# Kernel optimization log

Measured on AMD Instinct MI355X. Metric: run time of the kernel, lower is better.

The kernel has to match this reference:

```python
import jax, jax.numpy as jnp
import numpy as np

NEG = -1.0e9

def setup_inputs() -> dict:
    key = jax.random.key(0)
    kq, kk, kv = jax.random.split(key, 3)
    B, Sq, Sk, D = 8, 2048, 2048, 128
    q = jax.random.normal(kq, (B, Sq, D), dtype=jnp.float32)
    k = jax.random.normal(kk, (B, Sk, D), dtype=jnp.float32)
    v = jax.random.normal(kv, (B, Sk, D), dtype=jnp.float32)
    mask = jnp.ones((B, Sq, Sk), dtype=jnp.int32)  # 1 = attend
    return {"q": q, "k": k, "v": v, "mask": mask}

def reference(q, k, v, mask):
    # scaled scores: [B, Sq, Sk]
    temper = jnp.sqrt(jnp.asarray(k.shape[-1], dtype=q.dtype))
    attn = jnp.einsum('bqd,bkd->bqk', q, k) / temper
    # additive mask: -1e9 where mask == 0
    attn = attn + NEG * (1.0 - mask.astype(attn.dtype))
    attn = jax.nn.softmax(attn, axis=-1)
    # dropout rate 0.0 -> identity
    out = jnp.einsum('bqk,bkd->bqd', attn, v)
    return out, attn
```

## Files before the change

kernel.cpp:

```cpp
#include <hip/hip_runtime.h>
#include <hip/hip_bf16.h>

#define BB 8
#define SQ 2048
#define SK 2048
#define DD 128
#define INV_TEMPER 0.08838834764831845f

using s16x8 = __attribute__((ext_vector_type(8))) short;
using f32x4 = __attribute__((ext_vector_type(4))) float;

__device__ __forceinline__ unsigned short f2bf(float f) {
  union { float f; unsigned u; } v; v.f = f;
  unsigned r = v.u + 0x7FFFu + ((v.u >> 16) & 1u);
  return (unsigned short)(r >> 16);
}
__device__ __forceinline__ float bf2f(unsigned short h) {
  union { unsigned u; float f; } v; v.u = ((unsigned)h) << 16; return v.f;
}
__device__ __forceinline__ void bar_lds() {
  asm volatile("s_waitcnt lgkmcnt(0)" ::: "memory");
  __builtin_amdgcn_s_barrier();
}

__global__ __launch_bounds__(256) void prep_k_kernel(const float* __restrict__ k,
                                                     unsigned short* __restrict__ kb) {
  const size_t i = ((size_t)blockIdx.x * 256 + threadIdx.x) * 8;
  const float4 a = *(const float4*)(k + i);
  const float4 c = *(const float4*)(k + i + 4);
  ushort4 o0, o1;
  o0.x = f2bf(a.x); o0.y = f2bf(a.y); o0.z = f2bf(a.z); o0.w = f2bf(a.w);
  o1.x = f2bf(c.x); o1.y = f2bf(c.y); o1.z = f2bf(c.z); o1.w = f2bf(c.w);
  *(ushort4*)(kb + i) = o0;
  *(ushort4*)(kb + i + 4) = o1;
}

__global__ __launch_bounds__(256) void prep_v_kernel(const float* __restrict__ v,
                                                     unsigned short* __restrict__ vt) {
  constexpr int TS = 132;
  __shared__ __align__(16) unsigned short tile[64 * TS];
  const int tid = threadIdx.x;
  const int bid = blockIdx.x;
  const int b  = bid >> 5;
  const int k0 = (bid & 31) << 6;
#pragma unroll
  for (int p = 0; p < 8; ++p) {
    const int row = p * 8 + (tid >> 5);
    const int c4  = (tid & 31) << 2;
    const float4 vv = *(const float4*)(v + ((size_t)(b * SK + k0 + row)) * DD + c4);
    ushort4 o; o.x = f2bf(vv.x); o.y = f2bf(vv.y); o.z = f2bf(vv.z); o.w = f2bf(vv.w);
    *(ushort4*)(&tile[row * TS + c4]) = o;
  }
  __syncthreads();
#pragma unroll
  for (int p = 0; p < 8; ++p) {
    const int u = p * 256 + tid;
    const int d  = u >> 4;
    const int kw = (u & 15) << 2;
    ushort4 o;
    o.x = tile[(kw + 0) * TS + d];
    o.y = tile[(kw + 1) * TS + d];
    o.z = tile[(kw + 2) * TS + d];
    o.w = tile[(kw + 3) * TS + d];
    *(ushort4*)(vt + ((size_t)(b * DD + d)) * SK + k0 + kw) = o;
  }
}

__global__ __launch_bounds__(512, 4) void fused_attn(
    const float* __restrict__ q, const int* __restrict__ mask,
    const unsigned short* __restrict__ kb, const unsigned short* __restrict__ vt,
    float* __restrict__ outp, float* __restrict__ attn) {
  constexpr int BMS = 260;
  constexpr int LDP = 136;
  __shared__ unsigned char bm[32 * BMS];
  __shared__ __align__(16) unsigned short p_lds[2][32][LDP];
  __shared__ float redl[8][32];

  const int tid = threadIdx.x;
  const int bid = blockIdx.x;
  const int swz = ((bid & 7) << 6) + (bid >> 3);
  const int b  = swz >> 6;
  const int q0 = (swz & 63) << 5;
  const int lane = tid & 63;
  const int w    = tid >> 6;
  const int lrow = lane & 15;
  const int lk   = lane >> 4;
  const int colw = (w << 4) + lrow;
  const int cbyte = colw >> 3;
  const int cbit  = colw & 7;
  const int rowb  = lk << 2;

  {
    const int* mbase = mask + ((size_t)(b * SQ + q0)) * SK;
#pragma unroll
    for (int i = 0; i < 16; ++i) {
      const int u = (i << 9) + tid;
      const int grow = u >> 8;
      const int gb   = u & 255;
      const int* pp = mbase + (size_t)grow * SK + ((size_t)gb << 3);
      const int4 m0 = *(const int4*)pp;
      const int4 m1 = *(const int4*)(pp + 4);
      unsigned bv = (unsigned)(m0.x != 0) | ((unsigned)(m0.y != 0) << 1) |
                    ((unsigned)(m0.z != 0) << 2) | ((unsigned)(m0.w != 0) << 3) |
                    ((unsigned)(m1.x != 0) << 4) | ((unsigned)(m1.y != 0) << 5) |
                    ((unsigned)(m1.z != 0) << 6) | ((unsigned)(m1.w != 0) << 7);
      bm[grow * BMS + gb] = (unsigned char)bv;
    }
  }

  s16x8 af0[4], af1[4];
#pragma unroll
  for (int ks = 0; ks < 4; ++ks) {
    const float* qp0 = q + ((size_t)(b * SQ + q0 + lrow)) * DD + ks * 32 + lk * 8;
    const float* qp1 = qp0 + 16 * DD;
    const float4 a0 = *(const float4*)qp0;
    const float4 a1 = *(const float4*)(qp0 + 4);
    const float4 c0 = *(const float4*)qp1;
    const float4 c1 = *(const float4*)(qp1 + 4);
    s16x8 x, y;
    x[0] = (short)f2bf(a0.x); x[1] = (short)f2bf(a0.y); x[2] = (short)f2bf(a0.z); x[3] = (short)f2bf(a0.w);
    x[4] = (short)f2bf(a1.x); x[5] = (short)f2bf(a1.y); x[6] = (short)f2bf(a1.z); x[7] = (short)f2bf(a1.w);
    y[0] = (short)f2bf(c0.x); y[1] = (short)f2bf(c0.y); y[2] = (short)f2bf(c0.z); y[3] = (short)f2bf(c0.w);
    y[4] = (short)f2bf(c1.x); y[5] = (short)f2bf(c1.y); y[6] = (short)f2bf(c1.z); y[7] = (short)f2bf(c1.w);
    af0[ks] = x; af1[ks] = y;
  }

  const unsigned short* kbb = kb + (size_t)b * SK * DD + (size_t)colw * DD + lk * 8;

  bar_lds();

  float ls[8];
#pragma unroll
  for (int i = 0; i < 8; ++i) ls[i] = 0.0f;

  s16x8 bA[4], bB[4];
#pragma unroll
  for (int ks = 0; ks < 4; ++ks) bA[ks] = *(const s16x8*)(kbb + ks * 32);

  auto qk_sink1 = [&](int t, const f32x4& a0, const f32x4& a1) {
    const int bybase = (t << 4) + cbyte;
#pragma unroll
    for (int rt = 0; rt < 2; ++rt)
#pragma unroll
      for (int r = 0; r < 4; ++r) {
        const int row = rt * 16 + rowb + r;
        const int live = (bm[row * BMS + bybase] >> cbit) & 1;
        const float s = (rt ? a1[r] : a0[r]) * INV_TEMPER;
        ls[rt * 4 + r] += live ? __expf(s) : 0.0f;
      }
  };
  auto qk_mfma = [&](const s16x8* bf, f32x4& a0, f32x4& a1) {
    __builtin_amdgcn_s_setprio(1);
#pragma unroll
    for (int ks = 0; ks < 4; ++ks) {
      a0 = __builtin_amdgcn_mfma_f32_16x16x32_bf16(af0[ks], bf[ks], a0, 0, 0, 0);
      a1 = __builtin_amdgcn_mfma_f32_16x16x32_bf16(af1[ks], bf[ks], a1, 0, 0, 0);
    }
    __builtin_amdgcn_s_setprio(0);
  };

#pragma unroll 1
  for (int tp = 0; tp < 8; ++tp) {
    const int t0 = tp << 1, t1 = t0 + 1;
    {
      const unsigned short* p = kbb + (size_t)t1 * (128 * DD);
#pragma unroll
      for (int ks = 0; ks < 4; ++ks) bB[ks] = *(const s16x8*)(p + ks * 32);
    }
    f32x4 a0 = {0.f,0.f,0.f,0.f}, a1 = {0.f,0.f,0.f,0.f};
    qk_mfma(bA, a0, a1);
    qk_sink1(t0, a0, a1);
    {
      const int tn = (t0 + 2) & 15;
      const unsigned short* p = kbb + (size_t)tn * (128 * DD);
#pragma unroll
      for (int ks = 0; ks < 4; ++ks) bA[ks] = *(const s16x8*)(p + ks * 32);
    }
    f32x4 c0 = {0.f,0.f,0.f,0.f}, c1 = {0.f,0.f,0.f,0.f};
    qk_mfma(bB, c0, c1);
    qk_sink1(t1, c0, c1);
  }

#pragma unroll
  for (int i = 0; i < 8; ++i) {
    float l = ls[i];
#pragma unroll
    for (int d = 1; d < 16; d <<= 1) l += __shfl_xor(l, d);
    ls[i] = l;
  }
  if (lrow == 0) {
#pragma unroll
    for (int i = 0; i < 8; ++i) redl[w][(i >> 2) * 16 + rowb + (i & 3)] = ls[i];
  }
#pragma unroll
  for (int ks = 0; ks < 4; ++ks) bA[ks] = *(const s16x8*)(kbb + ks * 32);
  bar_lds();
  float il[8];
#pragma unroll
  for (int i = 0; i < 8; ++i) {
    const int row = (i >> 2) * 16 + rowb + (i & 3);
    float l = 0.0f;
#pragma unroll
    for (int ww = 0; ww < 8; ++ww) l += redl[ww][row];
    il[i] = 1.0f / l;
  }

  f32x4 o0 = {0.f,0.f,0.f,0.f}, o1 = {0.f,0.f,0.f,0.f};
  const unsigned short* vrow = vt + ((size_t)(b * DD + colw)) * SK + lk * 8;
  const int arow  = tid >> 4;
  const int acol0 = (tid & 15) << 3;
  float* attn_base = attn + ((size_t)(b * SQ + q0 + arow)) * SK + acol0;

  auto pv_iter = [&](int t, const s16x8* bcur, s16x8* bnx) {
    const int kr0 = t << 7;
    const int buf = t & 1;
    {
      const int tn = (t + 1) & 15;
      const unsigned short* p = kbb + (size_t)tn * (128 * DD);
#pragma unroll
      for (int ks = 0; ks < 4; ++ks) bnx[ks] = *(const s16x8*)(p + ks * 32);
    }
    s16x8 vf[4];
#pragma unroll
    for (int ks = 0; ks < 4; ++ks) vf[ks] = *(const s16x8*)(vrow + kr0 + ks * 32);
    f32x4 a0 = {0.f,0.f,0.f,0.f}, a1 = {0.f,0.f,0.f,0.f};
    qk_mfma(bcur, a0, a1);
    const int bybase = (t << 4) + cbyte;
#pragma unroll
    for (int rt = 0; rt < 2; ++rt)
#pragma unroll
      for (int r = 0; r < 4; ++r) {
        const int row = rt * 16 + rowb + r;
        const int live = (bm[row * BMS + bybase] >> cbit) & 1;
        const float s = (rt ? a1[r] : a0[r]) * INV_TEMPER;
        const float p = live ? __expf(s) * il[rt * 4 + r] : 0.0f;
        p_lds[buf][row][colw] = f2bf(p);
      }
    bar_lds();
    {
      const s16x8 pr = *(const s16x8*)(&p_lds[buf][arow][acol0]);
      float4 g0, g1;
      g0.x = bf2f((unsigned short)pr[0]); g0.y = bf2f((unsigned short)pr[1]);
      g0.z = bf2f((unsigned short)pr[2]); g0.w = bf2f((unsigned short)pr[3]);
      g1.x = bf2f((unsigned short)pr[4]); g1.y = bf2f((unsigned short)pr[5]);
      g1.z = bf2f((unsigned short)pr[6]); g1.w = bf2f((unsigned short)pr[7]);
      *(float4*)(attn_base + kr0) = g0;
      *(float4*)(attn_base + kr0 + 4) = g1;
    }
    __builtin_amdgcn_s_setprio(1);
#pragma unroll
    for (int ks = 0; ks < 4; ++ks) {
      const s16x8 pa0 = *(const s16x8*)(&p_lds[buf][lrow][ks * 32 + lk * 8]);
      const s16x8 pa1 = *(const s16x8*)(&p_lds[buf][16 + lrow][ks * 32 + lk * 8]);
      o0 = __builtin_amdgcn_mfma_f32_16x16x32_bf16(pa0, vf[ks], o0, 0, 0, 0);
      o1 = __builtin_amdgcn_mfma_f32_16x16x32_bf16(pa1, vf[ks], o1, 0, 0, 0);
    }
    __builtin_amdgcn_s_setprio(0);
  };

#pragma unroll 1
  for (int tp = 0; tp < 8; ++tp) {
    pv_iter((tp << 1),     bA, bB);
    pv_iter((tp << 1) + 1, bB, bA);
  }

#pragma unroll
  for (int rt = 0; rt < 2; ++rt)
#pragma unroll
    for (int r = 0; r < 4; ++r) {
      const int row = q0 + rt * 16 + rowb + r;
      outp[((size_t)(b * SQ + row)) * DD + colw] = (rt ? o1[r] : o0[r]);
    }
}

extern "C" void kernel_launch(void* const* d_in, const int* in_sizes, int n_in,
                              void* d_out, int out_size, void* d_ws, size_t ws_size,
                              hipStream_t stream) {
  const float* q = (const float*)d_in[0];
  const float* k = (const float*)d_in[1];
  const float* v = (const float*)d_in[2];
  const int* mask = (const int*)d_in[3];
  float* outp = (float*)d_out;
  float* attn = outp + (size_t)BB * SQ * DD;

  unsigned short* kb = (unsigned short*)d_ws;
  unsigned short* vt = kb + (size_t)BB * SK * DD;

  prep_k_kernel<<<(BB * SK * DD) / (256 * 8), 256, 0, stream>>>(k, kb);
  prep_v_kernel<<<BB * (SK / 64), 256, 0, stream>>>(v, vt);
  fused_attn<<<BB * (SQ / 32), 512, 0, stream>>>(q, mask, kb, vt, outp, attn);
}
```

Measured before the change: 140.7 us.

## Single-pass attention: store unnormalized P in LDS, split keys across waves

Replaces the two-pass scheme (sum of exponentials first, then recomputing QK^T for PV) with a single pass. Each wave owns a 256-key slice, writes unnormalized bf16 exp scores into a full 32x2048 LDS buffer and accumulates partial PV products. The partial outputs are reduced across waves with LDS atomics and normalized at the end, and the attention matrix is written from LDS with nontemporal stores. This removes the second QK^T matmul and the per-tile barriers. In exchange it needs much more LDS, so occupancy drops (launch bounds lowered to 2), and it relies on exp without max subtraction and on LDS float atomics.

Result: slower. 245.0 us (+74.1%).

```diff
diff --git a/kernel.cpp b/kernel.cpp
--- a/kernel.cpp
+++ b/kernel.cpp
@@ -9,6 +9,7 @@
 
 using s16x8 = __attribute__((ext_vector_type(8))) short;
 using f32x4 = __attribute__((ext_vector_type(4))) float;
+using i32x4 = __attribute__((ext_vector_type(4))) int;
 
 __device__ __forceinline__ unsigned short f2bf(float f) {
   union { float f; unsigned u; } v; v.f = f;
@@ -17,10 +18,6 @@
 }
 __device__ __forceinline__ float bf2f(unsigned short h) {
   union { unsigned u; float f; } v; v.u = ((unsigned)h) << 16; return v.f;
-}
-__device__ __forceinline__ void bar_lds() {
-  asm volatile("s_waitcnt lgkmcnt(0)" ::: "memory");
-  __builtin_amdgcn_s_barrier();
 }
 
 __global__ __launch_bounds__(256) void prep_k_kernel(const float* __restrict__ k,
@@ -66,15 +63,18 @@
   }
 }
 
-__global__ __launch_bounds__(512, 4) void fused_attn(
+#define PSTR 2056
+#define BMS  260
+
+__global__ __launch_bounds__(512, 2) void fused_attn(
     const float* __restrict__ q, const int* __restrict__ mask,
     const unsigned short* __restrict__ kb, const unsigned short* __restrict__ vt,
     float* __restrict__ outp, float* __restrict__ attn) {
-  constexpr int BMS = 260;
-  constexpr int LDP = 136;
+  __shared__ __align__(16) unsigned short P[32 * PSTR];
   __shared__ unsigned char bm[32 * BMS];
-  __shared__ __align__(16) unsigned short p_lds[2][32][LDP];
+  __shared__ float obuf[32 * 128];
   __shared__ float redl[8][32];
+  __shared__ float il_s[32];
 
   const int tid = threadIdx.x;
   const int bid = blockIdx.x;
@@ -85,10 +85,11 @@
   const int w    = tid >> 6;
   const int lrow = lane & 15;
   const int lk   = lane >> 4;
-  const int colw = (w << 4) + lrow;
-  const int cbyte = colw >> 3;
-  const int cbit  = colw & 7;
-  const int rowb  = lk << 2;
+  const int rowb = lk << 2;
+  const int slice0 = w << 8;
+
+#pragma unroll
+  for (int i = 0; i < 8; ++i) obuf[tid + (i << 9)] = 0.0f;
 
   {
     const int* mbase = mask + ((size_t)(b * SQ + q0)) * SK;
@@ -98,8 +99,8 @@
       const int grow = u >> 8;
       const int gb   = u & 255;
       const int* pp = mbase + (size_t)grow * SK + ((size_t)gb << 3);
-      const int4 m0 = *(const int4*)pp;
-      const int4 m1 = *(const int4*)(pp + 4);
+      const i32x4 m0 = __builtin_nontemporal_load((const i32x4*)pp);
+      const i32x4 m1 = __builtin_nontemporal_load(((const i32x4*)pp) + 1);
       unsigned bv = (unsigned)(m0.x != 0) | ((unsigned)(m0.y != 0) << 1) |
                     ((unsigned)(m0.z != 0) << 2) | ((unsigned)(m0.w != 0) << 3) |
                     ((unsigned)(m1.x != 0) << 4) | ((unsigned)(m1.y != 0) << 5) |
@@ -125,60 +126,73 @@
     af0[ks] = x; af1[ks] = y;
   }
 
-  const unsigned short* kbb = kb + (size_t)b * SK * DD + (size_t)colw * DD + lk * 8;
-
-  bar_lds();
+  __syncthreads();
+
+  const unsigned short* kfp = kb + (size_t)b * SK * DD + (size_t)(slice0 + lrow) * DD + lk * 8;
+  const unsigned short* vfp = vt + ((size_t)(b * DD + lrow)) * SK + slice0 + lk * 8;
 
   float ls[8];
 #pragma unroll
   for (int i = 0; i < 8; ++i) ls[i] = 0.0f;
-
-  s16x8 bA[4], bB[4];
-#pragma unroll
-  for (int ks = 0; ks < 4; ++ks) bA[ks] = *(const s16x8*)(kbb + ks * 32);
-
-  auto qk_sink1 = [&](int t, const f32x4& a0, const f32x4& a1) {
-    const int bybase = (t << 4) + cbyte;
+  f32x4 oA[8], oB[8];
+#pragma unroll
+  for (int nt = 0; nt < 8; ++nt) { oA[nt] = f32x4{0.f,0.f,0.f,0.f}; oB[nt] = f32x4{0.f,0.f,0.f,0.f}; }
+
+  auto qk_sink = [&](int ct, const s16x8* kf) {
+    f32x4 a0 = {0.f,0.f,0.f,0.f}, a1 = {0.f,0.f,0.f,0.f};
+    __builtin_amdgcn_s_setprio(1);
+#pragma unroll
+    for (int ks = 0; ks < 4; ++ks) {
+      a0 = __builtin_amdgcn_mfma_f32_16x16x32_bf16(af0[ks], kf[ks], a0, 0, 0, 0);
+      a1 = __builtin_amdgcn_mfma_f32_16x16x32_bf16(af1[ks], kf[ks], a1, 0, 0, 0);
+    }
+    __builtin_amdgcn_s_setprio(0);
+    const int colg = slice0 + (ct << 4) + lrow;
+    const int byb = colg >> 3, bit = colg & 7;
 #pragma unroll
     for (int rt = 0; rt < 2; ++rt)
 #pragma unroll
       for (int r = 0; r < 4; ++r) {
         const int row = rt * 16 + rowb + r;
-        const int live = (bm[row * BMS + bybase] >> cbit) & 1;
+        const int live = (bm[row * BMS + byb] >> bit) & 1;
         const float s = (rt ? a1[r] : a0[r]) * INV_TEMPER;
-        ls[rt * 4 + r] += live ? __expf(s) : 0.0f;
+        const float e = live ? __expf(s) : 0.0f;
+        ls[rt * 4 + r] += e;
+        P[row * PSTR + colg] = f2bf(e);
       }
   };
-  auto qk_mfma = [&](const s16x8* bf, f32x4& a0, f32x4& a1) {
+
+  s16x8 kA[4], kB[4];
+#pragma unroll
+  for (int ks = 0; ks < 4; ++ks) kA[ks] = *(const s16x8*)(kfp + ks * 32);
+
+#pragma unroll 1
+  for (int kk = 0; kk < 8; ++kk) {
+    const int koff = kk << 5;
+    s16x8 vf[8];
+#pragma unroll
+    for (int nt = 0; nt < 8; ++nt)
+      vf[nt] = *(const s16x8*)(vfp + (size_t)(nt << 4) * SK + koff);
+#pragma unroll
+    for (int ks = 0; ks < 4; ++ks)
+      kB[ks] = *(const s16x8*)(kfp + (size_t)(((kk << 1) + 1) << 4) * DD + ks * 32);
+    qk_sink(kk << 1, kA);
+#pragma unroll
+    for (int ks = 0; ks < 4; ++ks)
+      kA[ks] = *(const s16x8*)(kfp + (size_t)((((kk << 1) + 2) & 15) << 4) * DD + ks * 32);
+    qk_sink((kk << 1) + 1, kB);
+    asm volatile("s_waitcnt lgkmcnt(0)" ::: "memory");
+    __builtin_amdgcn_sched_barrier(0);
+    const int ko = slice0 + koff + (lk << 3);
+    const s16x8 pa0 = *(const s16x8*)(&P[lrow * PSTR + ko]);
+    const s16x8 pa1 = *(const s16x8*)(&P[(16 + lrow) * PSTR + ko]);
     __builtin_amdgcn_s_setprio(1);
 #pragma unroll
-    for (int ks = 0; ks < 4; ++ks) {
-      a0 = __builtin_amdgcn_mfma_f32_16x16x32_bf16(af0[ks], bf[ks], a0, 0, 0, 0);
-      a1 = __builtin_amdgcn_mfma_f32_16x16x32_bf16(af1[ks], bf[ks], a1, 0, 0, 0);
+    for (int nt = 0; nt < 8; ++nt) {
+      oA[nt] = __builtin_amdgcn_mfma_f32_16x16x32_bf16(pa0, vf[nt], oA[nt], 0, 0, 0);
+      oB[nt] = __builtin_amdgcn_mfma_f32_16x16x32_bf16(pa1, vf[nt], oB[nt], 0, 0, 0);
     }
     __builtin_amdgcn_s_setprio(0);
-  };
-
-#pragma unroll 1
-  for (int tp = 0; tp < 8; ++tp) {
-    const int t0 = tp << 1, t1 = t0 + 1;
-    {
-      const unsigned short* p = kbb + (size_t)t1 * (128 * DD);
-#pragma unroll
-      for (int ks = 0; ks < 4; ++ks) bB[ks] = *(const s16x8*)(p + ks * 32);
-    }
-    f32x4 a0 = {0.f,0.f,0.f,0.f}, a1 = {0.f,0.f,0.f,0.f};
-    qk_mfma(bA, a0, a1);
-    qk_sink1(t0, a0, a1);
-    {
-      const int tn = (t0 + 2) & 15;
-      const unsigned short* p = kbb + (size_t)tn * (128 * DD);
-#pragma unroll
-      for (int ks = 0; ks < 4; ++ks) bA[ks] = *(const s16x8*)(p + ks * 32);
-    }
-    f32x4 c0 = {0.f,0.f,0.f,0.f}, c1 = {0.f,0.f,0.f,0.f};
-    qk_mfma(bB, c0, c1);
-    qk_sink1(t1, c0, c1);
   }
 
 #pragma unroll
@@ -190,87 +204,53 @@
   }
   if (lrow == 0) {
 #pragma unroll
-    for (int i = 0; i < 8; ++i) redl[w][(i >> 2) * 16 + rowb + (i & 3)] = ls[i];
-  }
-#pragma unroll
-  for (int ks = 0; ks < 4; ++ks) bA[ks] = *(const s16x8*)(kbb + ks * 32);
-  bar_lds();
-  float il[8];
-#pragma unroll
-  for (int i = 0; i < 8; ++i) {
-    const int row = (i >> 2) * 16 + rowb + (i & 3);
-    float l = 0.0f;
-#pragma unroll
-    for (int ww = 0; ww < 8; ++ww) l += redl[ww][row];
-    il[i] = 1.0f / l;
-  }
-
-  f32x4 o0 = {0.f,0.f,0.f,0.f}, o1 = {0.f,0.f,0.f,0.f};
-  const unsigned short* vrow = vt + ((size_t)(b * DD + colw)) * SK + lk * 8;
-  const int arow  = tid >> 4;
-  const int acol0 = (tid & 15) << 3;
-  float* attn_base = attn + ((size_t)(b * SQ + q0 + arow)) * SK + acol0;
-
-  auto pv_iter = [&](int t, const s16x8* bcur, s16x8* bnx) {
-    const int kr0 = t << 7;
-    const int buf = t & 1;
-    {
-      const int tn = (t + 1) & 15;
-      const unsigned short* p = kbb + (size_t)tn * (128 * DD);
-#pragma unroll
-      for (int ks = 0; ks < 4; ++ks) bnx[ks] = *(const s16x8*)(p + ks * 32);
-    }
-    s16x8 vf[4];
-#pragma unroll
-    for (int ks = 0; ks < 4; ++ks) vf[ks] = *(const s16x8*)(vrow + kr0 + ks * 32);
-    f32x4 a0 = {0.f,0.f,0.f,0.f}, a1 = {0.f,0.f,0.f,0.f};
-    qk_mfma(bcur, a0, a1);
-    const int bybase = (t << 4) + cbyte;
-#pragma unroll
-    for (int rt = 0; rt < 2; ++rt)
-#pragma unroll
-      for (int r = 0; r < 4; ++r) {
-        const int row = rt * 16 + rowb + r;
-        const int live = (bm[row * BMS + bybase] >> cbit) & 1;
-        const float s = (rt ? a1[r] : a0[r]) * INV_TEMPER;
-        const float p = live ? __expf(s) * il[rt * 4 + r] : 0.0f;
-        p_lds[buf][row][colw] = f2bf(p);
-      }
-    bar_lds();
-    {
-      const s16x8 pr = *(const s16x8*)(&p_lds[buf][arow][acol0]);
-      float4 g0, g1;
-      g0.x = bf2f((unsigned short)pr[0]); g0.y = bf2f((unsigned short)pr[1]);
-      g0.z = bf2f((unsigned short)pr[2]); g0.w = bf2f((unsigned short)pr[3]);
-      g1.x = bf2f((unsigned short)pr[4]); g1.y = bf2f((unsigned short)pr[5]);
-      g1.z = bf2f((unsigned short)pr[6]); g1.w = bf2f((unsigned short)pr[7]);
-      *(float4*)(attn_base + kr0) = g0;
-      *(float4*)(attn_base + kr0 + 4) = g1;
-    }
-    __builtin_amdgcn_s_setprio(1);
-#pragma unroll
-    for (int ks = 0; ks < 4; ++ks) {
-      const s16x8 pa0 = *(const s16x8*)(&p_lds[buf][lrow][ks * 32 + lk * 8]);
-      const s16x8 pa1 = *(const s16x8*)(&p_lds[buf][16 + lrow][ks * 32 + lk * 8]);
-      o0 = __builtin_amdgcn_mfma_f32_16x16x32_bf16(pa0, vf[ks], o0, 0, 0, 0);
-      o1 = __builtin_amdgcn_mfma_f32_16x16x32_bf16(pa1, vf[ks], o1, 0, 0, 0);
-    }
-    __builtin_amdgcn_s_setprio(0);
-  };
-
-#pragma unroll 1
-  for (int tp = 0; tp < 8; ++tp) {
-    pv_iter((tp << 1),     bA, bB);
-    pv_iter((tp << 1) + 1, bB, bA);
-  }
-
-#pragma unroll
-  for (int rt = 0; rt < 2; ++rt)
+    for (int i = 0; i < 8; ++i)
+      redl[w][((i >> 2) << 4) + rowb + (i & 3)] = ls[i];
+  }
+  __syncthreads();
+  if (tid < 32) {
+    float l = 0.f;
+#pragma unroll
+    for (int ww = 0; ww < 8; ++ww) l += redl[ww][tid];
+    il_s[tid] = 1.0f / l;
+  }
+#pragma unroll
+  for (int nt = 0; nt < 8; ++nt)
 #pragma unroll
     for (int r = 0; r < 4; ++r) {
-      const int row = q0 + rt * 16 + rowb + r;
-      outp[((size_t)(b * SQ + row)) * DD + colw] = (rt ? o1[r] : o0[r]);
-    }
+      atomicAdd(&obuf[(rowb + r) * 128 + (nt << 4) + lrow], oA[nt][r]);
+      atomicAdd(&obuf[(16 + rowb + r) * 128 + (nt << 4) + lrow], oB[nt][r]);
+    }
+  __syncthreads();
+
+  const int orow = tid >> 4;
+  const int ocol = (tid & 15) << 3;
+  const float ilr = il_s[orow];
+
+  {
+    float4 u0, u1;
+    const float* ob = &obuf[orow * 128 + ocol];
+    u0.x = ob[0] * ilr; u0.y = ob[1] * ilr; u0.z = ob[2] * ilr; u0.w = ob[3] * ilr;
+    u1.x = ob[4] * ilr; u1.y = ob[5] * ilr; u1.z = ob[6] * ilr; u1.w = ob[7] * ilr;
+    float* op = outp + ((size_t)(b * SQ + q0 + orow)) * DD + ocol;
+    *(float4*)op = u0;
+    *(float4*)(op + 4) = u1;
+  }
+
+  float* abase = attn + ((size_t)(b * SQ + q0 + orow)) * SK;
+  const unsigned short* prow = &P[orow * PSTR];
+#pragma unroll 2
+  for (int i = 0; i < 16; ++i) {
+    const int c0 = (i << 7) + ocol;
+    const s16x8 pr = *(const s16x8*)(&prow[c0]);
+    f32x4 g0, g1;
+    g0[0] = bf2f((unsigned short)pr[0]) * ilr; g0[1] = bf2f((unsigned short)pr[1]) * ilr;
+    g0[2] = bf2f((unsigned short)pr[2]) * ilr; g0[3] = bf2f((unsigned short)pr[3]) * ilr;
+    g1[0] = bf2f((unsigned short)pr[4]) * ilr; g1[1] = bf2f((unsigned short)pr[5]) * ilr;
+    g1[2] = bf2f((unsigned short)pr[6]) * ilr; g1[3] = bf2f((unsigned short)pr[7]) * ilr;
+    __builtin_nontemporal_store(g0, (f32x4*)(abase + c0));
+    __builtin_nontemporal_store(g1, (f32x4*)(abase + c0 + 4));
+  }
 }
 
 extern "C" void kernel_launch(void* const* d_in, const int* in_sizes, int n_in,
```

## Split attention over key halves with mask bitpack prepass and exp2 scaling

Applied to the files above, without the earlier changes.

Merges the K/V prep kernels and adds a mask bit-packing pass using wave ballots, so the attention kernels read a compact bitmask instead of the int mask. The single fused kernel becomes two kernels, a row-sum pass and an emit pass, each splitting the key dimension into two halves to double the block count. The emit pass accumulates the output with atomics into a pre-zeroed buffer. K is prescaled by log2(e)/sqrt(d) so exp2f can replace the scaled expf. The cost is an extra memset and launch, QK recomputed across the two passes, and float atomics on the output.

Measured after the change: 383.8 us. +172.8%, slower.

```diff
diff --git a/kernel.cpp b/kernel.cpp
--- a/kernel.cpp
+++ b/kernel.cpp
@@ -5,7 +5,7 @@
 #define SQ 2048
 #define SK 2048
 #define DD 128
-#define INV_TEMPER 0.08838834764831845f
+#define KSCALE 0.12751649736401815f
 
 using s16x8 = __attribute__((ext_vector_type(8))) short;
 using f32x4 = __attribute__((ext_vector_type(4))) float;
@@ -23,89 +23,87 @@
   __builtin_amdgcn_s_barrier();
 }
 
-__global__ __launch_bounds__(256) void prep_k_kernel(const float* __restrict__ k,
-                                                     unsigned short* __restrict__ kb) {
-  const size_t i = ((size_t)blockIdx.x * 256 + threadIdx.x) * 8;
-  const float4 a = *(const float4*)(k + i);
-  const float4 c = *(const float4*)(k + i + 4);
-  ushort4 o0, o1;
-  o0.x = f2bf(a.x); o0.y = f2bf(a.y); o0.z = f2bf(a.z); o0.w = f2bf(a.w);
-  o1.x = f2bf(c.x); o1.y = f2bf(c.y); o1.z = f2bf(c.z); o1.w = f2bf(c.w);
-  *(ushort4*)(kb + i) = o0;
-  *(ushort4*)(kb + i + 4) = o1;
-}
-
-__global__ __launch_bounds__(256) void prep_v_kernel(const float* __restrict__ v,
-                                                     unsigned short* __restrict__ vt) {
-  constexpr int TS = 132;
-  __shared__ __align__(16) unsigned short tile[64 * TS];
+__global__ __launch_bounds__(256) void prep_all(
+    const float* __restrict__ k, const float* __restrict__ v,
+    const int* __restrict__ m, unsigned short* __restrict__ kb,
+    unsigned short* __restrict__ vt, unsigned long long* __restrict__ mb) {
+  const int bid = blockIdx.x;
+  const int tid = threadIdx.x;
+  if (bid < 1024) {
+    const size_t i = ((size_t)bid * 256 + tid) * 8;
+    const float4 a = *(const float4*)(k + i);
+    const float4 c = *(const float4*)(k + i + 4);
+    ushort4 o0, o1;
+    o0.x = f2bf(a.x * KSCALE); o0.y = f2bf(a.y * KSCALE);
+    o0.z = f2bf(a.z * KSCALE); o0.w = f2bf(a.w * KSCALE);
+    o1.x = f2bf(c.x * KSCALE); o1.y = f2bf(c.y * KSCALE);
+    o1.z = f2bf(c.z * KSCALE); o1.w = f2bf(c.w * KSCALE);
+    *(ushort4*)(kb + i) = o0;
+    *(ushort4*)(kb + i + 4) = o1;
+  } else if (bid < 1280) {
+    constexpr int TS = 132;
+    __shared__ __align__(16) unsigned short tile[64 * TS];
+    const int vb = bid - 1024;
+    const int b  = vb >> 5;
+    const int k0 = (vb & 31) << 6;
+#pragma unroll
+    for (int p = 0; p < 8; ++p) {
+      const int row = p * 8 + (tid >> 5);
+      const int c4  = (tid & 31) << 2;
+      const float4 vv = *(const float4*)(v + ((size_t)(b * SK + k0 + row)) * DD + c4);
+      ushort4 o; o.x = f2bf(vv.x); o.y = f2bf(vv.y); o.z = f2bf(vv.z); o.w = f2bf(vv.w);
+      *(ushort4*)(&tile[row * TS + c4]) = o;
+    }
+    __syncthreads();
+#pragma unroll
+    for (int p = 0; p < 8; ++p) {
+      const int u = p * 256 + tid;
+      const int d  = u >> 4;
+      const int kw = (u & 15) << 2;
+      ushort4 o;
+      o.x = tile[(kw + 0) * TS + d];
+      o.y = tile[(kw + 1) * TS + d];
+      o.z = tile[(kw + 2) * TS + d];
+      o.w = tile[(kw + 3) * TS + d];
+      *(ushort4*)(vt + ((size_t)(b * DD + d)) * SK + k0 + kw) = o;
+    }
+  } else {
+    const int gw = ((bid - 1280) * 256 + tid) >> 6;
+    const int lane = tid & 63;
+    const int* rp = m + (size_t)gw * SK;
+    unsigned long long* wp = mb + (size_t)gw * (SK / 64);
+#pragma unroll 4
+    for (int i = 0; i < 32; ++i) {
+      const int mv = rp[i * 64 + lane];
+      const unsigned long long bal = __ballot(mv != 0);
+      if (lane == 0) wp[i] = bal;
+    }
+  }
+}
+
+#define BMSR 136
+#define LDP  136
+
+__global__ __launch_bounds__(512, 8) void attn_lsum(
+    const float* __restrict__ q, const unsigned long long* __restrict__ mb,
+    const unsigned short* __restrict__ kb, float* __restrict__ lpart) {
+  __shared__ unsigned char bm[32 * BMSR];
+  __shared__ float redl[8][32];
   const int tid = threadIdx.x;
   const int bid = blockIdx.x;
-  const int b  = bid >> 5;
-  const int k0 = (bid & 31) << 6;
-#pragma unroll
-  for (int p = 0; p < 8; ++p) {
-    const int row = p * 8 + (tid >> 5);
-    const int c4  = (tid & 31) << 2;
-    const float4 vv = *(const float4*)(v + ((size_t)(b * SK + k0 + row)) * DD + c4);
-    ushort4 o; o.x = f2bf(vv.x); o.y = f2bf(vv.y); o.z = f2bf(vv.z); o.w = f2bf(vv.w);
-    *(ushort4*)(&tile[row * TS + c4]) = o;
-  }
-  __syncthreads();
-#pragma unroll
-  for (int p = 0; p < 8; ++p) {
-    const int u = p * 256 + tid;
-    const int d  = u >> 4;
-    const int kw = (u & 15) << 2;
-    ushort4 o;
-    o.x = tile[(kw + 0) * TS + d];
-    o.y = tile[(kw + 1) * TS + d];
-    o.z = tile[(kw + 2) * TS + d];
-    o.w = tile[(kw + 3) * TS + d];
-    *(ushort4*)(vt + ((size_t)(b * DD + d)) * SK + k0 + kw) = o;
-  }
-}
-
-__global__ __launch_bounds__(512, 4) void fused_attn(
-    const float* __restrict__ q, const int* __restrict__ mask,
-    const unsigned short* __restrict__ kb, const unsigned short* __restrict__ vt,
-    float* __restrict__ outp, float* __restrict__ attn) {
-  constexpr int BMS = 260;
-  constexpr int LDP = 136;
-  __shared__ unsigned char bm[32 * BMS];
-  __shared__ __align__(16) unsigned short p_lds[2][32][LDP];
-  __shared__ float redl[8][32];
-
-  const int tid = threadIdx.x;
-  const int bid = blockIdx.x;
-  const int swz = ((bid & 7) << 6) + (bid >> 3);
-  const int b  = swz >> 6;
-  const int q0 = (swz & 63) << 5;
-  const int lane = tid & 63;
-  const int w    = tid >> 6;
-  const int lrow = lane & 15;
-  const int lk   = lane >> 4;
+  const int swz = ((bid & 7) << 7) + (bid >> 3);
+  const int b  = swz >> 7;
+  const int h  = swz & 1;
+  const int q0 = ((swz >> 1) & 63) << 5;
+  const int k0 = h << 10;
+  const int lane = tid & 63, w = tid >> 6, lrow = lane & 15, lk = lane >> 4;
+  const int rowb = lk << 2;
   const int colw = (w << 4) + lrow;
-  const int cbyte = colw >> 3;
-  const int cbit  = colw & 7;
-  const int rowb  = lk << 2;
 
   {
-    const int* mbase = mask + ((size_t)(b * SQ + q0)) * SK;
-#pragma unroll
-    for (int i = 0; i < 16; ++i) {
-      const int u = (i << 9) + tid;
-      const int grow = u >> 8;
-      const int gb   = u & 255;
-      const int* pp = mbase + (size_t)grow * SK + ((size_t)gb << 3);
-      const int4 m0 = *(const int4*)pp;
-      const int4 m1 = *(const int4*)(pp + 4);
-      unsigned bv = (unsigned)(m0.x != 0) | ((unsigned)(m0.y != 0) << 1) |
-                    ((unsigned)(m0.z != 0) << 2) | ((unsigned)(m0.w != 0) << 3) |
-                    ((unsigned)(m1.x != 0) << 4) | ((unsigned)(m1.y != 0) << 5) |
-                    ((unsigned)(m1.z != 0) << 6) | ((unsigned)(m1.w != 0) << 7);
-      bm[grow * BMS + gb] = (unsigned char)bv;
-    }
+    const int row = tid >> 4, wd = tid & 15;
+    *(unsigned long long*)&bm[row * BMSR + (wd << 3)] =
+        mb[(size_t)(b * SQ + q0 + row) * 32 + h * 16 + wd];
   }
 
   s16x8 af0[4], af1[4];
@@ -125,60 +123,52 @@
     af0[ks] = x; af1[ks] = y;
   }
 
-  const unsigned short* kbb = kb + (size_t)b * SK * DD + (size_t)colw * DD + lk * 8;
-
-  bar_lds();
-
-  float ls[8];
-#pragma unroll
-  for (int i = 0; i < 8; ++i) ls[i] = 0.0f;
-
-  s16x8 bA[4], bB[4];
-#pragma unroll
-  for (int ks = 0; ks < 4; ++ks) bA[ks] = *(const s16x8*)(kbb + ks * 32);
-
-  auto qk_sink1 = [&](int t, const f32x4& a0, const f32x4& a1) {
-    const int bybase = (t << 4) + cbyte;
+  const unsigned short* kfp = kb + ((size_t)(b * SK + k0 + colw)) * DD + lk * 8;
+  __syncthreads();
+
+  float ls[8] = {0.f, 0.f, 0.f, 0.f, 0.f, 0.f, 0.f, 0.f};
+
+  auto qk8 = [&](const s16x8* kf, f32x4& a0, f32x4& a1) {
+    __builtin_amdgcn_s_setprio(1);
+#pragma unroll
+    for (int ks = 0; ks < 4; ++ks) {
+      a0 = __builtin_amdgcn_mfma_f32_16x16x32_bf16(af0[ks], kf[ks], a0, 0, 0, 0);
+      a1 = __builtin_amdgcn_mfma_f32_16x16x32_bf16(af1[ks], kf[ks], a1, 0, 0, 0);
+    }
+    __builtin_amdgcn_s_setprio(0);
+  };
+  auto sink = [&](int t, const f32x4& a0, const f32x4& a1) {
+    const int byb = (t << 4) + (colw >> 3);
+    const int bit = colw & 7;
 #pragma unroll
     for (int rt = 0; rt < 2; ++rt)
 #pragma unroll
       for (int r = 0; r < 4; ++r) {
         const int row = rt * 16 + rowb + r;
-        const int live = (bm[row * BMS + bybase] >> cbit) & 1;
-        const float s = (rt ? a1[r] : a0[r]) * INV_TEMPER;
-        ls[rt * 4 + r] += live ? __expf(s) : 0.0f;
+        const int live = (bm[row * BMSR + byb] >> bit) & 1;
+        const float e = exp2f(rt ? a1[r] : a0[r]);
+        ls[rt * 4 + r] += live ? e : 0.0f;
       }
   };
-  auto qk_mfma = [&](const s16x8* bf, f32x4& a0, f32x4& a1) {
-    __builtin_amdgcn_s_setprio(1);
-#pragma unroll
-    for (int ks = 0; ks < 4; ++ks) {
-      a0 = __builtin_amdgcn_mfma_f32_16x16x32_bf16(af0[ks], bf[ks], a0, 0, 0, 0);
-      a1 = __builtin_amdgcn_mfma_f32_16x16x32_bf16(af1[ks], bf[ks], a1, 0, 0, 0);
-    }
-    __builtin_amdgcn_s_setprio(0);
-  };
-
+
+  s16x8 kA[4], kB[4];
+#pragma unroll
+  for (int ks = 0; ks < 4; ++ks) kA[ks] = *(const s16x8*)(kfp + ks * 32);
 #pragma unroll 1
-  for (int tp = 0; tp < 8; ++tp) {
-    const int t0 = tp << 1, t1 = t0 + 1;
-    {
-      const unsigned short* p = kbb + (size_t)t1 * (128 * DD);
-#pragma unroll
-      for (int ks = 0; ks < 4; ++ks) bB[ks] = *(const s16x8*)(p + ks * 32);
-    }
+  for (int tp = 0; tp < 4; ++tp) {
+    const int t0 = tp << 1;
+#pragma unroll
+    for (int ks = 0; ks < 4; ++ks)
+      kB[ks] = *(const s16x8*)(kfp + (size_t)(t0 + 1) * (128 * DD) + ks * 32);
     f32x4 a0 = {0.f,0.f,0.f,0.f}, a1 = {0.f,0.f,0.f,0.f};
-    qk_mfma(bA, a0, a1);
-    qk_sink1(t0, a0, a1);
-    {
-      const int tn = (t0 + 2) & 15;
-      const unsigned short* p = kbb + (size_t)tn * (128 * DD);
-#pragma unroll
-      for (int ks = 0; ks < 4; ++ks) bA[ks] = *(const s16x8*)(p + ks * 32);
-    }
+    qk8(kA, a0, a1);
+    sink(t0, a0, a1);
+#pragma unroll
+    for (int ks = 0; ks < 4; ++ks)
+      kA[ks] = *(const s16x8*)(kfp + (size_t)((t0 + 2) & 7) * (128 * DD) + ks * 32);
     f32x4 c0 = {0.f,0.f,0.f,0.f}, c1 = {0.f,0.f,0.f,0.f};
-    qk_mfma(bB, c0, c1);
-    qk_sink1(t1, c0, c1);
+    qk8(kB, c0, c1);
+    sink(t0 + 1, c0, c1);
   }
 
 #pragma unroll
@@ -190,51 +180,103 @@
   }
   if (lrow == 0) {
 #pragma unroll
-    for (int i = 0; i < 8; ++i) redl[w][(i >> 2) * 16 + rowb + (i & 3)] = ls[i];
-  }
-#pragma unroll
-  for (int ks = 0; ks < 4; ++ks) bA[ks] = *(const s16x8*)(kbb + ks * 32);
-  bar_lds();
+    for (int i = 0; i < 8; ++i)
+      redl[w][((i >> 2) << 4) + rowb + (i & 3)] = ls[i];
+  }
+  __syncthreads();
+  if (tid < 32) {
+    float l = 0.f;
+#pragma unroll
+    for (int ww = 0; ww < 8; ++ww) l += redl[ww][tid];
+    lpart[(size_t)h * (BB * SQ) + (size_t)b * SQ + q0 + tid] = l;
+  }
+}
+
+__global__ __launch_bounds__(512, 8) void attn_emit(
+    const float* __restrict__ q, const unsigned long long* __restrict__ mb,
+    const unsigned short* __restrict__ kb, const unsigned short* __restrict__ vt,
+    const float* __restrict__ lpart, float* __restrict__ outp,
+    float* __restrict__ attn) {
+  __shared__ unsigned char bm[32 * BMSR];
+  __shared__ __align__(16) unsigned short p_lds[2][32][LDP];
+  __shared__ float il_s[32];
+  const int tid = threadIdx.x;
+  const int bid = blockIdx.x;
+  const int swz = ((bid & 7) << 7) + (bid >> 3);
+  const int b  = swz >> 7;
+  const int h  = swz & 1;
+  const int q0 = ((swz >> 1) & 63) << 5;
+  const int k0 = h << 10;
+  const int lane = tid & 63, w = tid >> 6, lrow = lane & 15, lk = lane >> 4;
+  const int rowb = lk << 2;
+  const int colw = (w << 4) + lrow;
+
+  {
+    const int row = tid >> 4, wd = tid & 15;
+    *(unsigned long long*)&bm[row * BMSR + (wd << 3)] =
+        mb[(size_t)(b * SQ + q0 + row) * 32 + h * 16 + wd];
+  }
+  if (tid < 32) {
+    const size_t idx = (size_t)b * SQ + q0 + tid;
+    il_s[tid] = 1.0f / (lpart[idx] + lpart[idx + (size_t)BB * SQ]);
+  }
+
+  s16x8 af0[4], af1[4];
+#pragma unroll
+  for (int ks = 0; ks < 4; ++ks) {
+    const float* qp0 = q + ((size_t)(b * SQ + q0 + lrow)) * DD + ks * 32 + lk * 8;
+    const float* qp1 = qp0 + 16 * DD;
+    const float4 a0 = *(const float4*)qp0;
+    const float4 a1 = *(const float4*)(qp0 + 4);
+    const float4 c0 = *(const float4*)qp1;
+    const float4 c1 = *(const float4*)(qp1 + 4);
+    s16x8 x, y;
+    x[0] = (short)f2bf(a0.x); x[1] = (short)f2bf(a0.y); x[2] = (short)f2bf(a0.z); x[3] = (short)f2bf(a0.w);
+    x[4] = (short)f2bf(a1.x); x[5] = (short)f2bf(a1.y); x[6] = (short)f2bf(a1.z); x[7] = (short)f2bf(a1.w);
+    y[0] = (short)f2bf(c0.x); y[1] = (short)f2bf(c0.y); y[2] = (short)f2bf(c0.z); y[3] = (short)f2bf(c0.w);
+    y[4] = (short)f2bf(c1.x); y[5] = (short)f2bf(c1.y); y[6] = (short)f2bf(c1.z); y[7] = (short)f2bf(c1.w);
+    af0[ks] = x; af1[ks] = y;
+  }
+
+  const unsigned short* kfp = kb + ((size_t)(b * SK + k0 + colw)) * DD + lk * 8;
+  __syncthreads();
+
   float il[8];
 #pragma unroll
-  for (int i = 0; i < 8; ++i) {
-    const int row = (i >> 2) * 16 + rowb + (i & 3);
-    float l = 0.0f;
-#pragma unroll
-    for (int ww = 0; ww < 8; ++ww) l += redl[ww][row];
-    il[i] = 1.0f / l;
-  }
+  for (int i = 0; i < 8; ++i)
+    il[i] = il_s[((i >> 2) << 4) + rowb + (i & 3)];
 
   f32x4 o0 = {0.f,0.f,0.f,0.f}, o1 = {0.f,0.f,0.f,0.f};
-  const unsigned short* vrow = vt + ((size_t)(b * DD + colw)) * SK + lk * 8;
-  const int arow  = tid >> 4;
+  const unsigned short* vbase = vt + ((size_t)(b * DD + colw)) * SK + k0 + lk * 8;
+  const int arow = tid >> 4;
   const int acol0 = (tid & 15) << 3;
-  float* attn_base = attn + ((size_t)(b * SQ + q0 + arow)) * SK + acol0;
-
-  auto pv_iter = [&](int t, const s16x8* bcur, s16x8* bnx) {
-    const int kr0 = t << 7;
+  float* abase = attn + ((size_t)(b * SQ + q0 + arow)) * SK + k0 + acol0;
+
+#pragma unroll 2
+  for (int t = 0; t < 8; ++t) {
     const int buf = t & 1;
-    {
-      const int tn = (t + 1) & 15;
-      const unsigned short* p = kbb + (size_t)tn * (128 * DD);
-#pragma unroll
-      for (int ks = 0; ks < 4; ++ks) bnx[ks] = *(const s16x8*)(p + ks * 32);
-    }
-    s16x8 vf[4];
-#pragma unroll
-    for (int ks = 0; ks < 4; ++ks) vf[ks] = *(const s16x8*)(vrow + kr0 + ks * 32);
+    s16x8 kf[4];
+#pragma unroll
+    for (int ks = 0; ks < 4; ++ks)
+      kf[ks] = *(const s16x8*)(kfp + (size_t)t * (128 * DD) + ks * 32);
     f32x4 a0 = {0.f,0.f,0.f,0.f}, a1 = {0.f,0.f,0.f,0.f};
-    qk_mfma(bcur, a0, a1);
-    const int bybase = (t << 4) + cbyte;
+    __builtin_amdgcn_s_setprio(1);
+#pragma unroll
+    for (int ks = 0; ks < 4; ++ks) {
+      a0 = __builtin_amdgcn_mfma_f32_16x16x32_bf16(af0[ks], kf[ks], a0, 0, 0, 0);
+      a1 = __builtin_amdgcn_mfma_f32_16x16x32_bf16(af1[ks], kf[ks], a1, 0, 0, 0);
+    }
+    __builtin_amdgcn_s_setprio(0);
+    const int byb = (t << 4) + (colw >> 3);
+    const int bit = colw & 7;
 #pragma unroll
     for (int rt = 0; rt < 2; ++rt)
 #pragma unroll
       for (int r = 0; r < 4; ++r) {
         const int row = rt * 16 + rowb + r;
-        const int live = (bm[row * BMS + bybase] >> cbit) & 1;
-        const float s = (rt ? a1[r] : a0[r]) * INV_TEMPER;
-        const float p = live ? __expf(s) * il[rt * 4 + r] : 0.0f;
-        p_lds[buf][row][colw] = f2bf(p);
+        const int live = (bm[row * BMSR + byb] >> bit) & 1;
+        const float e = exp2f(rt ? a1[r] : a0[r]) * il[rt * 4 + r];
+        p_lds[buf][row][colw] = f2bf(live ? e : 0.0f);
       }
     bar_lds();
     {
@@ -244,24 +286,20 @@
       g0.z = bf2f((unsigned short)pr[2]); g0.w = bf2f((unsigned short)pr[3]);
       g1.x = bf2f((unsigned short)pr[4]); g1.y = bf2f((unsigned short)pr[5]);
       g1.z = bf2f((unsigned short)pr[6]); g1.w = bf2f((unsigned short)pr[7]);
-      *(float4*)(attn_base + kr0) = g0;
-      *(float4*)(attn_base + kr0 + 4) = g1;
+      float* ap = abase + (t << 7);
+      *(float4*)ap = g0;
+      *(float4*)(ap + 4) = g1;
     }
     __builtin_amdgcn_s_setprio(1);
 #pragma unroll
     for (int ks = 0; ks < 4; ++ks) {
       const s16x8 pa0 = *(const s16x8*)(&p_lds[buf][lrow][ks * 32 + lk * 8]);
       const s16x8 pa1 = *(const s16x8*)(&p_lds[buf][16 + lrow][ks * 32 + lk * 8]);
-      o0 = __builtin_amdgcn_mfma_f32_16x16x32_bf16(pa0, vf[ks], o0, 0, 0, 0);
-      o1 = __builtin_amdgcn_mfma_f32_16x16x32_bf16(pa1, vf[ks], o1, 0, 0, 0);
+      const s16x8 vf = *(const s16x8*)(vbase + (t << 7) + ks * 32);
+      o0 = __builtin_amdgcn_mfma_f32_16x16x32_bf16(pa0, vf, o0, 0, 0, 0);
+      o1 = __builtin_amdgcn_mfma_f32_16x16x32_bf16(pa1, vf, o1, 0, 0, 0);
     }
     __builtin_amdgcn_s_setprio(0);
-  };
-
-#pragma unroll 1
-  for (int tp = 0; tp < 8; ++tp) {
-    pv_iter((tp << 1),     bA, bB);
-    pv_iter((tp << 1) + 1, bB, bA);
   }
 
 #pragma unroll
@@ -269,7 +307,7 @@
 #pragma unroll
     for (int r = 0; r < 4; ++r) {
       const int row = q0 + rt * 16 + rowb + r;
-      outp[((size_t)(b * SQ + row)) * DD + colw] = (rt ? o1[r] : o0[r]);
+      atomicAdd(outp + ((size_t)(b * SQ + row)) * DD + colw, rt ? o1[r] : o0[r]);
     }
 }
 
@@ -285,8 +323,11 @@
 
   unsigned short* kb = (unsigned short*)d_ws;
   unsigned short* vt = kb + (size_t)BB * SK * DD;
-
-  prep_k_kernel<<<(BB * SK * DD) / (256 * 8), 256, 0, stream>>>(k, kb);
-  prep_v_kernel<<<BB * (SK / 64), 256, 0, stream>>>(v, vt);
-  fused_attn<<<BB * (SQ / 32), 512, 0, stream>>>(q, mask, kb, vt, outp, attn);
-}
+  unsigned long long* mbits = (unsigned long long*)(vt + (size_t)BB * SK * DD);
+  float* lpart = (float*)(mbits + (size_t)BB * SQ * (SK / 64));
+
+  hipMemsetAsync(outp, 0, (size_t)BB * SQ * DD * sizeof(float), stream);
+  prep_all<<<1024 + 256 + 4096, 256, 0, stream>>>(k, v, mask, kb, vt, mbits);
+  attn_lsum<<<1024, 512, 0, stream>>>(q, mbits, kb, lpart);
+  attn_emit<<<1024, 512, 0, stream>>>(q, mbits, kb, vt, lpart, outp, attn);
+}
```
